# Optimization experiments

Hardware: AMD Instinct MI355X
Metric: run time of the kernel (lower is better)

Reference implementation:

```python
import jax, jax.numpy as jnp
import numpy as np

BN_EPS = 1e-5


def setup_inputs() -> dict:
    key = jax.random.key(0)
    ks = jax.random.split(key, 8)
    bs, N, J, F_in, F_out = 8, 1024, 3, 32, 64
    num_inputs = J * F_in          # 96
    h1 = F_out // 2                # fc1 out
    h2 = F_out - h1                # fc2 out
    WW = jax.random.normal(ks[0], (bs, N, N, J), dtype=jnp.float32)
    x = jax.random.normal(ks[1], (bs, N, F_in), dtype=jnp.float32)
    s = 1.0 / np.sqrt(num_inputs)
    W1 = jax.random.uniform(ks[2], (h1, num_inputs), minval=-s, maxval=s, dtype=jnp.float32)
    b1 = jax.random.uniform(ks[3], (h1,), minval=-s, maxval=s, dtype=jnp.float32)
    W2 = jax.random.uniform(ks[4], (h2, num_inputs), minval=-s, maxval=s, dtype=jnp.float32)
    b2 = jax.random.uniform(ks[5], (h2,), minval=-s, maxval=s, dtype=jnp.float32)
    gamma = jnp.ones((F_out,), dtype=jnp.float32)
    beta = jnp.zeros((F_out,), dtype=jnp.float32)
    return {"WW": WW, "x": x, "W1": W1, "b1": b1, "W2": W2, "b2": b2,
            "gamma": gamma, "beta": beta}


def reference(WW, x, W1, b1, W2, b2, gamma, beta):
    bs, N, _, J = WW.shape
    # GMul: split/cat/bmm chain is equivalent to a single einsum.
    # out[b,n,j,f] = sum_m W[b,n,m,j] * x[b,m,f]; cat order -> (bs, N, J*F)
    y = jnp.einsum('bnmj,bmf->bnjf', WW, x).reshape(bs * N, J * x.shape[-1])
    x1 = jax.nn.relu(y @ W1.T + b1)
    x2 = y @ W2.T + b2
    z = jnp.concatenate([x1, x2], axis=1)           # (bs*N, F_out)
    # BatchNorm1d in training mode: biased batch statistics over bs*N rows
    mean = jnp.mean(z, axis=0)
    var = jnp.var(z, axis=0)
    z = (z - mean) * jax.lax.rsqrt(var + BN_EPS) * gamma + beta
    return z.reshape(bs, N, -1)
```

## Files before the change

### kernel.cpp

```cpp
#include <hip/hip_runtime.h>

typedef __attribute__((ext_vector_type(8))) short bh8;
typedef __attribute__((ext_vector_type(4))) float fx4;

__device__ __forceinline__ unsigned short f2bf(float f) {
  unsigned u = __float_as_uint(f);
  u += 0x7FFFu + ((u >> 16) & 1u);
  return (unsigned short)(u >> 16);
}

__device__ __forceinline__ bh8 pack8(float4 u, float4 v) {
  bh8 r;
  r[0] = (short)f2bf(u.x); r[1] = (short)f2bf(u.y);
  r[2] = (short)f2bf(u.z); r[3] = (short)f2bf(u.w);
  r[4] = (short)f2bf(v.x); r[5] = (short)f2bf(v.y);
  r[6] = (short)f2bf(v.z); r[7] = (short)f2bf(v.w);
  return r;
}

__global__ void __launch_bounds__(256) k0_bt(const float* __restrict__ x,
    const float* __restrict__ W1, const float* __restrict__ W2,
    unsigned short* __restrict__ bt) {
  __shared__ float xl[32][32];
  __shared__ float wl[96][64];
  int t = threadIdx.x;
  int bid = blockIdx.x;
  int b = bid >> 5, c = bid & 31;

  for (int i = t; i < 3072; i += 256) {
    int r = i / 96, k = i - r * 96;
    wl[k][r]      = W1[i];
    wl[k][r + 32] = W2[i];
  }
  const float4* xs = (const float4*)(x + (size_t)(b * 1024 + c * 32) * 32);
  ((float4*)xl)[t] = xs[t];
  __syncthreads();

  int o = t & 63;
  int q = t >> 6;
  int m0 = q * 8;
  float acc[8][3];
#pragma unroll
  for (int m = 0; m < 8; ++m) acc[m][0] = acc[m][1] = acc[m][2] = 0.f;
#pragma unroll
  for (int f4 = 0; f4 < 8; ++f4) {
    float wv[3][4];
#pragma unroll
    for (int u = 0; u < 4; ++u) {
      int f = f4 * 4 + u;
      wv[0][u] = wl[f][o];
      wv[1][u] = wl[32 + f][o];
      wv[2][u] = wl[64 + f][o];
    }
#pragma unroll
    for (int m = 0; m < 8; ++m) {
      float4 xv = *(const float4*)&xl[m0 + m][f4 * 4];
#pragma unroll
      for (int j = 0; j < 3; ++j) {
        acc[m][j] = fmaf(xv.x, wv[j][0], acc[m][j]);
        acc[m][j] = fmaf(xv.y, wv[j][1], acc[m][j]);
        acc[m][j] = fmaf(xv.z, wv[j][2], acc[m][j]);
        acc[m][j] = fmaf(xv.w, wv[j][3], acc[m][j]);
      }
    }
  }
  unsigned pk[12];
#pragma unroll
  for (int i = 0; i < 12; ++i) {
    unsigned short lo = f2bf(acc[(2 * i) / 3][(2 * i) % 3]);
    unsigned short hi = f2bf(acc[(2 * i + 1) / 3][(2 * i + 1) % 3]);
    pk[i] = (unsigned)lo | ((unsigned)hi << 16);
  }
  unsigned short* orow = bt + (size_t)(b * 64 + o) * 3072;
  uint4* op = (uint4*)(orow + 3 * (c * 32 + m0));
  op[0] = make_uint4(pk[0], pk[1], pk[2], pk[3]);
  op[1] = make_uint4(pk[4], pk[5], pk[6], pk[7]);
  op[2] = make_uint4(pk[8], pk[9], pk[10], pk[11]);
}

__global__ void __launch_bounds__(256) k1_gemm(const float* __restrict__ A,
    const unsigned short* __restrict__ BT, float* __restrict__ parts) {
  int t = threadIdx.x;
  int w = t >> 6, l = t & 63;
  int lr = l & 15, lg = l >> 4;
  int bid = blockIdx.x;
  int ks = bid & 7, mt = bid >> 3;
  int arow = mt * 64 + w * 16 + lr;
  int b = mt >> 4;
  int kbase = ks * 384 + lg * 8;
  const float* ap = A + (size_t)arow * 3072 + kbase;
  const unsigned short* bp = BT + (size_t)b * 196608 + (size_t)lr * 3072 + kbase;

  fx4 acc0 = {0.f,0.f,0.f,0.f}, acc1 = {0.f,0.f,0.f,0.f};
  fx4 acc2 = {0.f,0.f,0.f,0.f}, acc3 = {0.f,0.f,0.f,0.f};

#define LOADA_(s, ra, rb) { ra = *(const float4*)(ap + (s) * 32); \
                            rb = *(const float4*)(ap + (s) * 32 + 4); }
#define LOADB_(s, c0, c1, c2, c3) { \
    c0 = *(const bh8*)(bp + (s) * 32); \
    c1 = *(const bh8*)(bp + 49152 + (s) * 32); \
    c2 = *(const bh8*)(bp + 98304 + (s) * 32); \
    c3 = *(const bh8*)(bp + 147456 + (s) * 32); }
#define STEP_(ra, rb, c0, c1, c2, c3) { bh8 av = pack8(ra, rb); \
    acc0 = __builtin_amdgcn_mfma_f32_16x16x32_bf16(av, c0, acc0, 0, 0, 0); \
    acc1 = __builtin_amdgcn_mfma_f32_16x16x32_bf16(av, c1, acc1, 0, 0, 0); \
    acc2 = __builtin_amdgcn_mfma_f32_16x16x32_bf16(av, c2, acc2, 0, 0, 0); \
    acc3 = __builtin_amdgcn_mfma_f32_16x16x32_bf16(av, c3, acc3, 0, 0, 0); }

  float4 aA0, aA1, aB0, aB1;
  bh8 bA0, bA1, bA2, bA3, bB0, bB1, bB2, bB3;
  LOADA_(0, aA0, aA1); LOADB_(0, bA0, bA1, bA2, bA3);
  LOADA_(1, aB0, aB1); LOADB_(1, bB0, bB1, bB2, bB3);
#pragma unroll
  for (int s = 0; s < 12; s += 2) {
    STEP_(aA0, aA1, bA0, bA1, bA2, bA3);
    if (s + 2 < 12) { LOADA_(s + 2, aA0, aA1); LOADB_(s + 2, bA0, bA1, bA2, bA3); }
    STEP_(aB0, aB1, bB0, bB1, bB2, bB3);
    if (s + 3 < 12) { LOADA_(s + 3, aB0, aB1); LOADB_(s + 3, bB0, bB1, bB2, bB3); }
  }
#undef LOADA_
#undef LOADB_
#undef STEP_

  float* pout = parts + ((size_t)ks * 8192 + (size_t)mt * 64 + w * 16) * 64;
#pragma unroll
  for (int r = 0; r < 4; ++r) {
    int ro = (lg * 4 + r) * 64 + lr;
    pout[ro]      = acc0[r];
    pout[ro + 16] = acc1[r];
    pout[ro + 32] = acc2[r];
    pout[ro + 48] = acc3[r];
  }
}

__global__ void __launch_bounds__(256) k2_red(const float* __restrict__ parts,
    const float* __restrict__ b1, const float* __restrict__ b2,
    float* __restrict__ z, float2* __restrict__ part2) {
  __shared__ float4 redA[4][16], redB[4][16];
  int t = threadIdx.x, bid = blockIdx.x;
  int w = t >> 6, l = t & 63;
  int o0 = (t & 15) * 4;
  float4 bias = (o0 < 32) ? ((const float4*)b1)[o0 >> 2]
                          : ((const float4*)b2)[(o0 - 32) >> 2];
  bool rl = (o0 < 32);
  float4 s1 = {0.f, 0.f, 0.f, 0.f}, s2 = {0.f, 0.f, 0.f, 0.f};
  const float4* p0 = (const float4*)parts;
#pragma unroll
  for (int kk = 0; kk < 4; ++kk) {
    int i4 = bid * 1024 + kk * 256 + t;
    float4 v = p0[i4];
#pragma unroll
    for (int j = 1; j < 8; ++j) {
      float4 vj = p0[j * 131072 + i4];
      v.x += vj.x; v.y += vj.y; v.z += vj.z; v.w += vj.w;
    }
    v.x += bias.x; v.y += bias.y; v.z += bias.z; v.w += bias.w;
    if (rl) {
      v.x = fmaxf(v.x, 0.f); v.y = fmaxf(v.y, 0.f);
      v.z = fmaxf(v.z, 0.f); v.w = fmaxf(v.w, 0.f);
    }
    ((float4*)z)[i4] = v;
    s1.x += v.x; s1.y += v.y; s1.z += v.z; s1.w += v.w;
    s2.x += v.x * v.x; s2.y += v.y * v.y; s2.z += v.z * v.z; s2.w += v.w * v.w;
  }
#define RED_(c) { s1.c += __shfl_xor(s1.c, 16); s1.c += __shfl_xor(s1.c, 32); \
                  s2.c += __shfl_xor(s2.c, 16); s2.c += __shfl_xor(s2.c, 32); }
  RED_(x) RED_(y) RED_(z) RED_(w)
#undef RED_
  if (l < 16) { redA[w][l] = s1; redB[w][l] = s2; }
  __syncthreads();
  if (t < 16) {
    float4 S = redA[0][t], Q = redB[0][t];
#pragma unroll
    for (int wv = 1; wv < 4; ++wv) {
      float4 a = redA[wv][t], q = redB[wv][t];
      S.x += a.x; S.y += a.y; S.z += a.z; S.w += a.w;
      Q.x += q.x; Q.y += q.y; Q.z += q.z; Q.w += q.w;
    }
    int ob = bid * 64 + t * 4;
    part2[ob + 0] = make_float2(S.x, Q.x);
    part2[ob + 1] = make_float2(S.y, Q.y);
    part2[ob + 2] = make_float2(S.z, Q.z);
    part2[ob + 3] = make_float2(S.w, Q.w);
  }
}

__global__ void k3_stats(const float2* __restrict__ part2, const float* __restrict__ gamma,
                         const float* __restrict__ beta, float2* __restrict__ stats) {
  __shared__ float red[2][4][64];
  int t = threadIdx.x;
  int o = t & 63, c = t >> 6;
  float S = 0.f, Q = 0.f;
#pragma unroll 4
  for (int i = 0; i < 32; ++i) {
    float2 p = part2[(c * 32 + i) * 64 + o];
    S += p.x; Q += p.y;
  }
  red[0][c][o] = S; red[1][c][o] = Q;
  __syncthreads();
  if (t < 64) {
    float Ss = 0.f, Qs = 0.f;
#pragma unroll
    for (int cc = 0; cc < 4; ++cc) { Ss += red[0][cc][t]; Qs += red[1][cc][t]; }
    float mean = Ss * (1.0f / 8192.0f);
    float var = fmaxf(Qs * (1.0f / 8192.0f) - mean * mean, 0.f);
    float rstd = rsqrtf(var + 1e-5f);
    float scale = gamma[t] * rstd;
    stats[t] = make_float2(scale, beta[t] - mean * scale);
  }
}

__global__ void k4_norm(float* __restrict__ z, const float2* __restrict__ stats) {
  int i4 = blockIdx.x * 256 + threadIdx.x;
  float4 v = ((const float4*)z)[i4];
  int o0 = (i4 & 15) * 4;
  float2 s0 = stats[o0 + 0], s1 = stats[o0 + 1], s2 = stats[o0 + 2], s3 = stats[o0 + 3];
  v.x = v.x * s0.x + s0.y;
  v.y = v.y * s1.x + s1.y;
  v.z = v.z * s2.x + s2.y;
  v.w = v.w * s3.x + s3.y;
  ((float4*)z)[i4] = v;
}

extern "C" void kernel_launch(void* const* d_in, const int* in_sizes, int n_in,
                              void* d_out, int out_size, void* d_ws, size_t ws_size,
                              hipStream_t stream) {
  const float* WW = (const float*)d_in[0];
  const float* x  = (const float*)d_in[1];
  const float* W1 = (const float*)d_in[2];
  const float* b1 = (const float*)d_in[3];
  const float* W2 = (const float*)d_in[4];
  const float* b2 = (const float*)d_in[5];
  const float* gamma = (const float*)d_in[6];
  const float* beta  = (const float*)d_in[7];

  unsigned short* bt = (unsigned short*)d_ws;
  float*  parts = (float*)((char*)d_ws + 3145728);
  float2* part2 = (float2*)((char*)d_ws + 3145728 + 16777216);
  float2* stats = (float2*)((char*)d_ws + 3145728 + 16777216 + 65536);
  float* z = (float*)d_out;

  hipLaunchKernelGGL(k0_bt,    dim3(256),  dim3(256), 0, stream, x, W1, W2, bt);
  hipLaunchKernelGGL(k1_gemm,  dim3(1024), dim3(256), 0, stream, WW, bt, parts);
  hipLaunchKernelGGL(k2_red,   dim3(128),  dim3(256), 0, stream, parts, b1, b2, z, part2);
  hipLaunchKernelGGL(k3_stats, dim3(1),    dim3(256), 0, stream, part2, gamma, beta, stats);
  hipLaunchKernelGGL(k4_norm,  dim3(512),  dim3(256), 0, stream, z, stats);
}
```

Measured before the change: 194.5 us.

## Stage GEMM operands through LDS with async loads; fuse stats into norm kernel

```diff
diff --git a/kernel.cpp b/kernel.cpp
--- a/kernel.cpp
+++ b/kernel.cpp
@@ -18,9 +18,15 @@
   return r;
 }
 
+__device__ __forceinline__ void async_g2l16(const void* g, void* l) {
+  __builtin_amdgcn_global_load_lds(
+      (const __attribute__((address_space(1))) unsigned int*)g,
+      (__attribute__((address_space(3))) unsigned int*)l, 16, 0, 0);
+}
+
 __global__ void __launch_bounds__(256) k0_bt(const float* __restrict__ x,
     const float* __restrict__ W1, const float* __restrict__ W2,
-    unsigned short* __restrict__ bt) {
+    unsigned char* __restrict__ bt) {
   __shared__ float xl[32][32];
   __shared__ float wl[96][64];
   int t = threadIdx.x;
@@ -71,56 +77,88 @@
     unsigned short hi = f2bf(acc[(2 * i + 1) / 3][(2 * i + 1) % 3]);
     pk[i] = (unsigned)lo | ((unsigned)hi << 16);
   }
-  unsigned short* orow = bt + (size_t)(b * 64 + o) * 3072;
-  uint4* op = (uint4*)(orow + 3 * (c * 32 + m0));
-  op[0] = make_uint4(pk[0], pk[1], pk[2], pk[3]);
-  op[1] = make_uint4(pk[4], pk[5], pk[6], pk[7]);
-  op[2] = make_uint4(pk[8], pk[9], pk[10], pk[11]);
-}
-
-__global__ void __launch_bounds__(256) k1_gemm(const float* __restrict__ A,
-    const unsigned short* __restrict__ BT, float* __restrict__ parts) {
+  int ks = c >> 2;
+  int kb = (c & 3) * 192 + q * 48;
+  int swz = (o & 7) << 4;
+  unsigned char* ob = bt + (size_t)(b * 8 + ks) * 49152 + (size_t)o * 768;
+  *(uint4*)(ob + ((kb     ) ^ swz)) = make_uint4(pk[0], pk[1], pk[2],  pk[3]);
+  *(uint4*)(ob + ((kb + 16) ^ swz)) = make_uint4(pk[4], pk[5], pk[6],  pk[7]);
+  *(uint4*)(ob + ((kb + 32) ^ swz)) = make_uint4(pk[8], pk[9], pk[10], pk[11]);
+}
+
+__global__ void __launch_bounds__(256, 2) k1_gemm(const float* __restrict__ A,
+    const unsigned char* __restrict__ BTS, float* __restrict__ parts) {
+  __shared__ __align__(16) unsigned char smem[81920];
   int t = threadIdx.x;
   int w = t >> 6, l = t & 63;
   int lr = l & 15, lg = l >> 4;
   int bid = blockIdx.x;
   int ks = bid & 7, mt = bid >> 3;
-  int arow = mt * 64 + w * 16 + lr;
   int b = mt >> 4;
-  int kbase = ks * 384 + lg * 8;
-  const float* ap = A + (size_t)arow * 3072 + kbase;
-  const unsigned short* bp = BT + (size_t)b * 196608 + (size_t)lr * 3072 + kbase;
+  int r0 = mt * 64;
+
+  const unsigned char* bsrc = BTS + (size_t)(b * 8 + ks) * 49152 + w * 1024 + l * 16;
+#pragma unroll
+  for (int i = 0; i < 12; ++i)
+    async_g2l16(bsrc + i * 4096, smem + 32768 + i * 4096 + w * 1024);
+
+  int arow = w * 8 + (l >> 3);
+  int insw = ((l & 7) ^ (l >> 3)) << 4;
+  const unsigned char* ab = (const unsigned char*)(A + (size_t)r0 * 3072 + ks * 384);
+  const unsigned char* asrc0 = ab + (size_t)arow * 12288 + insw;
+  const unsigned char* asrc1 = ab + (size_t)(arow + 32) * 12288 + insw;
+
+#define STAGE_A(S) { \
+    unsigned char* sl = smem + ((S) & 3) * 8192 + w * 1024; \
+    async_g2l16(asrc0 + (S) * 128, sl); \
+    async_g2l16(asrc1 + (S) * 128, sl + 4096); }
 
   fx4 acc0 = {0.f,0.f,0.f,0.f}, acc1 = {0.f,0.f,0.f,0.f};
   fx4 acc2 = {0.f,0.f,0.f,0.f}, acc3 = {0.f,0.f,0.f,0.f};
 
-#define LOADA_(s, ra, rb) { ra = *(const float4*)(ap + (s) * 32); \
-                            rb = *(const float4*)(ap + (s) * 32 + 4); }
-#define LOADB_(s, c0, c1, c2, c3) { \
-    c0 = *(const bh8*)(bp + (s) * 32); \
-    c1 = *(const bh8*)(bp + 49152 + (s) * 32); \
-    c2 = *(const bh8*)(bp + 98304 + (s) * 32); \
-    c3 = *(const bh8*)(bp + 147456 + (s) * 32); }
-#define STEP_(ra, rb, c0, c1, c2, c3) { bh8 av = pack8(ra, rb); \
-    acc0 = __builtin_amdgcn_mfma_f32_16x16x32_bf16(av, c0, acc0, 0, 0, 0); \
-    acc1 = __builtin_amdgcn_mfma_f32_16x16x32_bf16(av, c1, acc1, 0, 0, 0); \
-    acc2 = __builtin_amdgcn_mfma_f32_16x16x32_bf16(av, c2, acc2, 0, 0, 0); \
-    acc3 = __builtin_amdgcn_mfma_f32_16x16x32_bf16(av, c3, acc3, 0, 0, 0); }
-
-  float4 aA0, aA1, aB0, aB1;
-  bh8 bA0, bA1, bA2, bA3, bB0, bB1, bB2, bB3;
-  LOADA_(0, aA0, aA1); LOADB_(0, bA0, bA1, bA2, bA3);
-  LOADA_(1, aB0, aB1); LOADB_(1, bB0, bB1, bB2, bB3);
-#pragma unroll
-  for (int s = 0; s < 12; s += 2) {
-    STEP_(aA0, aA1, bA0, bA1, bA2, bA3);
-    if (s + 2 < 12) { LOADA_(s + 2, aA0, aA1); LOADB_(s + 2, bA0, bA1, bA2, bA3); }
-    STEP_(aB0, aB1, bB0, bB1, bB2, bB3);
-    if (s + 3 < 12) { LOADA_(s + 3, aB0, aB1); LOADB_(s + 3, bB0, bB1, bB2, bB3); }
-  }
-#undef LOADA_
-#undef LOADB_
-#undef STEP_
+  int rb  = (w * 16 + lr) * 128;
+  int asw = (lr & 7) << 4;
+  const unsigned char* bl = smem + 32768 + lr * 768;
+
+#define READ_MFMA(S) { \
+    const unsigned char* sl = smem + ((S) & 3) * 8192; \
+    float4 a0 = *(const float4*)(sl + rb + ((lg * 32     ) ^ asw)); \
+    float4 a1 = *(const float4*)(sl + rb + ((lg * 32 + 16) ^ asw)); \
+    bh8 av = pack8(a0, a1); \
+    int kb = (S) * 64 + lg * 16; \
+    bh8 b0 = *(const bh8*)(bl +     0 + (kb ^ asw)); \
+    bh8 b1 = *(const bh8*)(bl + 12288 + (kb ^ asw)); \
+    bh8 b2 = *(const bh8*)(bl + 24576 + (kb ^ asw)); \
+    bh8 b3 = *(const bh8*)(bl + 36864 + (kb ^ asw)); \
+    acc0 = __builtin_amdgcn_mfma_f32_16x16x32_bf16(av, b0, acc0, 0, 0, 0); \
+    acc1 = __builtin_amdgcn_mfma_f32_16x16x32_bf16(av, b1, acc1, 0, 0, 0); \
+    acc2 = __builtin_amdgcn_mfma_f32_16x16x32_bf16(av, b2, acc2, 0, 0, 0); \
+    acc3 = __builtin_amdgcn_mfma_f32_16x16x32_bf16(av, b3, acc3, 0, 0, 0); }
+
+#define KSTEP_S(S, NW) { \
+    STAGE_A(S + 2); \
+    asm volatile("s_waitcnt vmcnt(" #NW ")" ::: "memory"); \
+    __builtin_amdgcn_s_barrier(); \
+    __builtin_amdgcn_sched_barrier(0); \
+    READ_MFMA(S); }
+
+#define KSTEP_N(S, NW) { \
+    asm volatile("s_waitcnt vmcnt(" #NW ")" ::: "memory"); \
+    __builtin_amdgcn_s_barrier(); \
+    __builtin_amdgcn_sched_barrier(0); \
+    READ_MFMA(S); }
+
+  STAGE_A(0);
+  STAGE_A(1);
+
+  KSTEP_S(0, 4)  KSTEP_S(1, 4)  KSTEP_S(2, 4)  KSTEP_S(3, 4)
+  KSTEP_S(4, 4)  KSTEP_S(5, 4)  KSTEP_S(6, 4)  KSTEP_S(7, 4)
+  KSTEP_S(8, 4)  KSTEP_S(9, 4)  KSTEP_N(10, 2) KSTEP_N(11, 0)
+
+#undef STAGE_A
+#undef READ_MFMA
+#undef KSTEP_S
+#undef KSTEP_N
 
   float* pout = parts + ((size_t)ks * 8192 + (size_t)mt * 64 + w * 16) * 64;
 #pragma unroll
@@ -185,10 +223,12 @@
   }
 }
 
-__global__ void k3_stats(const float2* __restrict__ part2, const float* __restrict__ gamma,
-                         const float* __restrict__ beta, float2* __restrict__ stats) {
+__global__ void __launch_bounds__(256) k4_norm(const float2* __restrict__ part2,
+    const float* __restrict__ gamma, const float* __restrict__ beta,
+    float* __restrict__ z) {
   __shared__ float red[2][4][64];
-  int t = threadIdx.x;
+  __shared__ float2 sstat[64];
+  int t = threadIdx.x, bid = blockIdx.x;
   int o = t & 63, c = t >> 6;
   float S = 0.f, Q = 0.f;
 #pragma unroll 4
@@ -206,20 +246,21 @@
     float var = fmaxf(Qs * (1.0f / 8192.0f) - mean * mean, 0.f);
     float rstd = rsqrtf(var + 1e-5f);
     float scale = gamma[t] * rstd;
-    stats[t] = make_float2(scale, beta[t] - mean * scale);
-  }
-}
-
-__global__ void k4_norm(float* __restrict__ z, const float2* __restrict__ stats) {
-  int i4 = blockIdx.x * 256 + threadIdx.x;
-  float4 v = ((const float4*)z)[i4];
-  int o0 = (i4 & 15) * 4;
-  float2 s0 = stats[o0 + 0], s1 = stats[o0 + 1], s2 = stats[o0 + 2], s3 = stats[o0 + 3];
-  v.x = v.x * s0.x + s0.y;
-  v.y = v.y * s1.x + s1.y;
-  v.z = v.z * s2.x + s2.y;
-  v.w = v.w * s3.x + s3.y;
-  ((float4*)z)[i4] = v;
+    sstat[t] = make_float2(scale, beta[t] - mean * scale);
+  }
+  __syncthreads();
+  int o0 = (t & 15) * 4;
+  float2 s0 = sstat[o0], s1 = sstat[o0 + 1], s2 = sstat[o0 + 2], s3 = sstat[o0 + 3];
+#pragma unroll
+  for (int k = 0; k < 4; ++k) {
+    int i4 = bid * 1024 + k * 256 + t;
+    float4 v = ((const float4*)z)[i4];
+    v.x = v.x * s0.x + s0.y;
+    v.y = v.y * s1.x + s1.y;
+    v.z = v.z * s2.x + s2.y;
+    v.w = v.w * s3.x + s3.y;
+    ((float4*)z)[i4] = v;
+  }
 }
 
 extern "C" void kernel_launch(void* const* d_in, const int* in_sizes, int n_in,
@@ -234,15 +275,13 @@
   const float* gamma = (const float*)d_in[6];
   const float* beta  = (const float*)d_in[7];
 
-  unsigned short* bt = (unsigned short*)d_ws;
+  unsigned char* bt = (unsigned char*)d_ws;
   float*  parts = (float*)((char*)d_ws + 3145728);
   float2* part2 = (float2*)((char*)d_ws + 3145728 + 16777216);
-  float2* stats = (float2*)((char*)d_ws + 3145728 + 16777216 + 65536);
   float* z = (float*)d_out;
 
-  hipLaunchKernelGGL(k0_bt,    dim3(256),  dim3(256), 0, stream, x, W1, W2, bt);
-  hipLaunchKernelGGL(k1_gemm,  dim3(1024), dim3(256), 0, stream, WW, bt, parts);
-  hipLaunchKernelGGL(k2_red,   dim3(128),  dim3(256), 0, stream, parts, b1, b2, z, part2);
-  hipLaunchKernelGGL(k3_stats, dim3(1),    dim3(256), 0, stream, part2, gamma, beta, stats);
-  hipLaunchKernelGGL(k4_norm,  dim3(512),  dim3(256), 0, stream, z, stats);
-}
+  hipLaunchKernelGGL(k0_bt,   dim3(256),  dim3(256), 0, stream, x, W1, W2, bt);
+  hipLaunchKernelGGL(k1_gemm, dim3(1024), dim3(256), 0, stream, WW, bt, parts);
+  hipLaunchKernelGGL(k2_red,  dim3(128),  dim3(256), 0, stream, parts, b1, b2, z, part2);
+  hipLaunchKernelGGL(k4_norm, dim3(128),  dim3(256), 0, stream, part2, gamma, beta, z);
+}
```

Result: faster. 184.7 us (-5.0%).

## Tile the bf16 B operand per k-chunk and fuse BN stats via atomics

Applied to the files above, without the earlier changes.

```diff
diff --git a/kernel.cpp b/kernel.cpp
--- a/kernel.cpp
+++ b/kernel.cpp
@@ -20,12 +20,14 @@
 
 __global__ void __launch_bounds__(256) k0_bt(const float* __restrict__ x,
     const float* __restrict__ W1, const float* __restrict__ W2,
-    unsigned short* __restrict__ bt) {
+    unsigned* __restrict__ btw, float* __restrict__ gstat) {
   __shared__ float xl[32][32];
   __shared__ float wl[96][64];
   int t = threadIdx.x;
   int bid = blockIdx.x;
   int b = bid >> 5, c = bid & 31;
+
+  if (bid == 0 && t < 128) gstat[t] = 0.f;
 
   for (int i = t; i < 3072; i += 256) {
     int r = i / 96, k = i - r * 96;
@@ -71,25 +73,26 @@
     unsigned short hi = f2bf(acc[(2 * i + 1) / 3][(2 * i + 1) % 3]);
     pk[i] = (unsigned)lo | ((unsigned)hi << 16);
   }
-  unsigned short* orow = bt + (size_t)(b * 64 + o) * 3072;
-  uint4* op = (uint4*)(orow + 3 * (c * 32 + m0));
-  op[0] = make_uint4(pk[0], pk[1], pk[2], pk[3]);
-  op[1] = make_uint4(pk[4], pk[5], pk[6], pk[7]);
-  op[2] = make_uint4(pk[8], pk[9], pk[10], pk[11]);
+  int kbase = 96 * c + 24 * q;
+#pragma unroll
+  for (int i = 0; i < 12; ++i) {
+    int kg = kbase + 2 * i;
+    int kc = kg >> 5, ki = kg & 31;
+    btw[((b * 96 + kc) * 64 + o) * 16 + (ki >> 1)] = pk[i];
+  }
 }
 
 __global__ void __launch_bounds__(256) k1_gemm(const float* __restrict__ A,
-    const unsigned short* __restrict__ BT, float* __restrict__ parts) {
+    const unsigned short* __restrict__ BT2, float* __restrict__ parts) {
   int t = threadIdx.x;
   int w = t >> 6, l = t & 63;
   int lr = l & 15, lg = l >> 4;
   int bid = blockIdx.x;
-  int ks = bid & 7, mt = bid >> 3;
-  int arow = mt * 64 + w * 16 + lr;
-  int b = mt >> 4;
-  int kbase = ks * 384 + lg * 8;
-  const float* ap = A + (size_t)arow * 3072 + kbase;
-  const unsigned short* bp = BT + (size_t)b * 196608 + (size_t)lr * 3072 + kbase;
+  int ks = bid & 7, mtb = bid >> 3;
+  int b = mtb >> 4;
+  int r0 = mtb * 64 + w * 16;
+  const float* ap = A + (size_t)(r0 + lr) * 3072 + ks * 384 + lg * 8;
+  const unsigned short* bp = BT2 + ((size_t)(b * 96 + ks * 12) * 64 + lr) * 32 + lg * 8;
 
   fx4 acc0 = {0.f,0.f,0.f,0.f}, acc1 = {0.f,0.f,0.f,0.f};
   fx4 acc2 = {0.f,0.f,0.f,0.f}, acc3 = {0.f,0.f,0.f,0.f};
@@ -97,10 +100,10 @@
 #define LOADA_(s, ra, rb) { ra = *(const float4*)(ap + (s) * 32); \
                             rb = *(const float4*)(ap + (s) * 32 + 4); }
 #define LOADB_(s, c0, c1, c2, c3) { \
-    c0 = *(const bh8*)(bp + (s) * 32); \
-    c1 = *(const bh8*)(bp + 49152 + (s) * 32); \
-    c2 = *(const bh8*)(bp + 98304 + (s) * 32); \
-    c3 = *(const bh8*)(bp + 147456 + (s) * 32); }
+    c0 = *(const bh8*)(bp + (s) * 2048); \
+    c1 = *(const bh8*)(bp + (s) * 2048 + 512); \
+    c2 = *(const bh8*)(bp + (s) * 2048 + 1024); \
+    c3 = *(const bh8*)(bp + (s) * 2048 + 1536); }
 #define STEP_(ra, rb, c0, c1, c2, c3) { bh8 av = pack8(ra, rb); \
     acc0 = __builtin_amdgcn_mfma_f32_16x16x32_bf16(av, c0, acc0, 0, 0, 0); \
     acc1 = __builtin_amdgcn_mfma_f32_16x16x32_bf16(av, c1, acc1, 0, 0, 0); \
@@ -122,7 +125,7 @@
 #undef LOADB_
 #undef STEP_
 
-  float* pout = parts + ((size_t)ks * 8192 + (size_t)mt * 64 + w * 16) * 64;
+  float* pout = parts + ((size_t)ks * 8192 + (size_t)r0) * 64;
 #pragma unroll
   for (int r = 0; r < 4; ++r) {
     int ro = (lg * 4 + r) * 64 + lr;
@@ -135,7 +138,7 @@
 
 __global__ void __launch_bounds__(256) k2_red(const float* __restrict__ parts,
     const float* __restrict__ b1, const float* __restrict__ b2,
-    float* __restrict__ z, float2* __restrict__ part2) {
+    float* __restrict__ z, float* __restrict__ gstat) {
   __shared__ float4 redA[4][16], redB[4][16];
   int t = threadIdx.x, bid = blockIdx.x;
   int w = t >> 6, l = t & 63;
@@ -143,26 +146,22 @@
   float4 bias = (o0 < 32) ? ((const float4*)b1)[o0 >> 2]
                           : ((const float4*)b2)[(o0 - 32) >> 2];
   bool rl = (o0 < 32);
-  float4 s1 = {0.f, 0.f, 0.f, 0.f}, s2 = {0.f, 0.f, 0.f, 0.f};
   const float4* p0 = (const float4*)parts;
-#pragma unroll
-  for (int kk = 0; kk < 4; ++kk) {
-    int i4 = bid * 1024 + kk * 256 + t;
-    float4 v = p0[i4];
-#pragma unroll
-    for (int j = 1; j < 8; ++j) {
-      float4 vj = p0[j * 131072 + i4];
-      v.x += vj.x; v.y += vj.y; v.z += vj.z; v.w += vj.w;
-    }
-    v.x += bias.x; v.y += bias.y; v.z += bias.z; v.w += bias.w;
-    if (rl) {
-      v.x = fmaxf(v.x, 0.f); v.y = fmaxf(v.y, 0.f);
-      v.z = fmaxf(v.z, 0.f); v.w = fmaxf(v.w, 0.f);
-    }
-    ((float4*)z)[i4] = v;
-    s1.x += v.x; s1.y += v.y; s1.z += v.z; s1.w += v.w;
-    s2.x += v.x * v.x; s2.y += v.y * v.y; s2.z += v.z * v.z; s2.w += v.w * v.w;
-  }
+  int i4 = bid * 256 + t;
+  float4 v = p0[i4];
+#pragma unroll
+  for (int j = 1; j < 8; ++j) {
+    float4 vj = p0[j * 131072 + i4];
+    v.x += vj.x; v.y += vj.y; v.z += vj.z; v.w += vj.w;
+  }
+  v.x += bias.x; v.y += bias.y; v.z += bias.z; v.w += bias.w;
+  if (rl) {
+    v.x = fmaxf(v.x, 0.f); v.y = fmaxf(v.y, 0.f);
+    v.z = fmaxf(v.z, 0.f); v.w = fmaxf(v.w, 0.f);
+  }
+  ((float4*)z)[i4] = v;
+  float4 s1 = v;
+  float4 s2 = make_float4(v.x * v.x, v.y * v.y, v.z * v.z, v.w * v.w);
 #define RED_(c) { s1.c += __shfl_xor(s1.c, 16); s1.c += __shfl_xor(s1.c, 32); \
                   s2.c += __shfl_xor(s2.c, 16); s2.c += __shfl_xor(s2.c, 32); }
   RED_(x) RED_(y) RED_(z) RED_(w)
@@ -177,44 +176,31 @@
       S.x += a.x; S.y += a.y; S.z += a.z; S.w += a.w;
       Q.x += q.x; Q.y += q.y; Q.z += q.z; Q.w += q.w;
     }
-    int ob = bid * 64 + t * 4;
-    part2[ob + 0] = make_float2(S.x, Q.x);
-    part2[ob + 1] = make_float2(S.y, Q.y);
-    part2[ob + 2] = make_float2(S.z, Q.z);
-    part2[ob + 3] = make_float2(S.w, Q.w);
-  }
-}
-
-__global__ void k3_stats(const float2* __restrict__ part2, const float* __restrict__ gamma,
-                         const float* __restrict__ beta, float2* __restrict__ stats) {
-  __shared__ float red[2][4][64];
-  int t = threadIdx.x;
-  int o = t & 63, c = t >> 6;
-  float S = 0.f, Q = 0.f;
-#pragma unroll 4
-  for (int i = 0; i < 32; ++i) {
-    float2 p = part2[(c * 32 + i) * 64 + o];
-    S += p.x; Q += p.y;
-  }
-  red[0][c][o] = S; red[1][c][o] = Q;
-  __syncthreads();
+    int ob = t * 4;
+    atomicAdd(&gstat[ob + 0], S.x); atomicAdd(&gstat[64 + ob + 0], Q.x);
+    atomicAdd(&gstat[ob + 1], S.y); atomicAdd(&gstat[64 + ob + 1], Q.y);
+    atomicAdd(&gstat[ob + 2], S.z); atomicAdd(&gstat[64 + ob + 2], Q.z);
+    atomicAdd(&gstat[ob + 3], S.w); atomicAdd(&gstat[64 + ob + 3], Q.w);
+  }
+}
+
+__global__ void __launch_bounds__(256) k4_norm(const float* __restrict__ gstat,
+    const float* __restrict__ gamma, const float* __restrict__ beta,
+    float* __restrict__ z) {
+  __shared__ float2 sstat[64];
+  int t = threadIdx.x, bid = blockIdx.x;
   if (t < 64) {
-    float Ss = 0.f, Qs = 0.f;
-#pragma unroll
-    for (int cc = 0; cc < 4; ++cc) { Ss += red[0][cc][t]; Qs += red[1][cc][t]; }
-    float mean = Ss * (1.0f / 8192.0f);
-    float var = fmaxf(Qs * (1.0f / 8192.0f) - mean * mean, 0.f);
+    float mean = gstat[t] * (1.0f / 8192.0f);
+    float var = fmaxf(gstat[64 + t] * (1.0f / 8192.0f) - mean * mean, 0.f);
     float rstd = rsqrtf(var + 1e-5f);
     float scale = gamma[t] * rstd;
-    stats[t] = make_float2(scale, beta[t] - mean * scale);
-  }
-}
-
-__global__ void k4_norm(float* __restrict__ z, const float2* __restrict__ stats) {
-  int i4 = blockIdx.x * 256 + threadIdx.x;
+    sstat[t] = make_float2(scale, beta[t] - mean * scale);
+  }
+  __syncthreads();
+  int i4 = bid * 256 + t;
+  int o0 = (t & 15) * 4;
+  float2 s0 = sstat[o0], s1 = sstat[o0 + 1], s2 = sstat[o0 + 2], s3 = sstat[o0 + 3];
   float4 v = ((const float4*)z)[i4];
-  int o0 = (i4 & 15) * 4;
-  float2 s0 = stats[o0 + 0], s1 = stats[o0 + 1], s2 = stats[o0 + 2], s3 = stats[o0 + 3];
   v.x = v.x * s0.x + s0.y;
   v.y = v.y * s1.x + s1.y;
   v.z = v.z * s2.x + s2.y;
@@ -235,14 +221,14 @@
   const float* beta  = (const float*)d_in[7];
 
   unsigned short* bt = (unsigned short*)d_ws;
-  float*  parts = (float*)((char*)d_ws + 3145728);
-  float2* part2 = (float2*)((char*)d_ws + 3145728 + 16777216);
-  float2* stats = (float2*)((char*)d_ws + 3145728 + 16777216 + 65536);
+  float* parts = (float*)((char*)d_ws + 3145728);
+  float* gstat = (float*)((char*)d_ws + 3145728 + 16777216);
   float* z = (float*)d_out;
 
-  hipLaunchKernelGGL(k0_bt,    dim3(256),  dim3(256), 0, stream, x, W1, W2, bt);
-  hipLaunchKernelGGL(k1_gemm,  dim3(1024), dim3(256), 0, stream, WW, bt, parts);
-  hipLaunchKernelGGL(k2_red,   dim3(128),  dim3(256), 0, stream, parts, b1, b2, z, part2);
-  hipLaunchKernelGGL(k3_stats, dim3(1),    dim3(256), 0, stream, part2, gamma, beta, stats);
-  hipLaunchKernelGGL(k4_norm,  dim3(512),  dim3(256), 0, stream, z, stats);
-}
+  hipLaunchKernelGGL(k0_bt,   dim3(256),  dim3(256), 0, stream, x, W1, W2,
+                     (unsigned*)bt, gstat);
+  hipLaunchKernelGGL(k1_gemm, dim3(1024), dim3(256), 0, stream, WW,
+                     (const unsigned short*)bt, parts);
+  hipLaunchKernelGGL(k2_red,  dim3(512),  dim3(256), 0, stream, parts, b1, b2, z, gstat);
+  hipLaunchKernelGGL(k4_norm, dim3(512),  dim3(256), 0, stream, gstat, gamma, beta, z);
+}
```

New measurement: 235.0 us. +20.8%, slower.
